# Performance work log

Hardware: AMD Instinct MI355X
Metric: run time of the kernel (lower is better)

## Reference

```python
import jax, jax.numpy as jnp
import numpy as np

GROUPS = 8
HEADS = 8
EPS = 1e-5


def setup_inputs() -> dict:
    key = jax.random.key(0)
    ks = jax.random.split(key, 4)
    B, C, T = 4, 512, 2048
    x = jax.random.normal(ks[0], (B, C, T), dtype=jnp.float32)
    gn_w = jnp.ones((C,), dtype=jnp.float32)
    gn_b = jnp.zeros((C,), dtype=jnp.float32)
    qkv_w = jax.random.normal(ks[1], (3 * C, C), dtype=jnp.float32) * (1.0 / np.sqrt(C))
    qkv_b = jnp.zeros((3 * C,), dtype=jnp.float32)
    proj_w = jax.random.normal(ks[2], (C, C), dtype=jnp.float32) * (1.0 / np.sqrt(C))
    proj_b = jnp.zeros((C,), dtype=jnp.float32)
    return {"x": x, "gn_w": gn_w, "gn_b": gn_b, "qkv_w": qkv_w,
            "qkv_b": qkv_b, "proj_w": proj_w, "proj_b": proj_b}


def reference(x, gn_w, gn_b, qkv_w, qkv_b, proj_w, proj_b):
    b, c, t = x.shape
    # GroupNorm over (channels_in_group, T)
    xg = x.reshape(b, GROUPS, c // GROUPS, t)
    mean = xg.mean(axis=(2, 3), keepdims=True)
    var = xg.var(axis=(2, 3), keepdims=True)
    h = ((xg - mean) * jax.lax.rsqrt(var + EPS)).reshape(b, c, t)
    h = h * gn_w[None, :, None] + gn_b[None, :, None]
    # 1x1 conv qkv: [b, 3c, t]
    qkv = jnp.einsum('oc,bct->bot', qkv_w, h) + qkv_b[None, :, None]
    # split into heads: legacy layout [b*H, 3*ch, t] -> q,k,v each [b*H, ch, t]
    ch = c // HEADS
    qkv = qkv.reshape(b * HEADS, 3 * ch, t)
    q, k, v = qkv[:, :ch], qkv[:, ch:2 * ch], qkv[:, 2 * ch:]
    scale = 1.0 / np.sqrt(np.sqrt(ch))
    weight = jnp.einsum('bct,bcs->bts', q * scale, k * scale)  # [bH, t, t]
    weight = jax.nn.softmax(weight.astype(jnp.float32), axis=-1).astype(q.dtype)
    a = jnp.einsum('bts,bcs->bct', weight, v).reshape(b, c, t)
    # 1x1 conv proj
    out = jnp.einsum('oc,bct->bot', proj_w, a) + proj_b[None, :, None]
    return x + out
```

## Files before the change

### kernel.cpp

```cpp
#include <hip/hip_runtime.h>


typedef __attribute__((ext_vector_type(8))) short short8;
typedef __attribute__((ext_vector_type(4))) float f32x4;
typedef __attribute__((ext_vector_type(16))) float f32x16;

#define T_DIM 2048
#define C_DIM 512
#define B_DIM 4

__device__ __forceinline__ float bf2f(ushort u) {
  union { unsigned int i; float f; } x; x.i = ((unsigned int)u) << 16; return x.f;
}
__device__ __forceinline__ ushort f2bf(float f) {
  union { float f; unsigned int i; } x; x.f = f;
  unsigned int i = x.i;
  return (ushort)((i + 0x7FFFu + ((i >> 16) & 1u)) >> 16);
}
__device__ __forceinline__ unsigned int cvtpk_bf16(float lo, float hi) {
  unsigned int r;
  asm("v_cvt_pk_bf16_f32 %0, %1, %2" : "=v"(r) : "v"(lo), "v"(hi));
  return r;
}
__device__ __forceinline__ float exp2_raw(float x) {
  float r;
  asm("v_exp_f32 %0, %1" : "=v"(r) : "v"(x));
  return r;
}
__device__ __forceinline__ void gl_lds16(const ushort* g, const ushort* l) {
  __builtin_amdgcn_global_load_lds(
      (const __attribute__((address_space(1))) unsigned int*)g,
      (__attribute__((address_space(3))) unsigned int*)l, 16, 0, 0);
}

#define KT_SCALE 0.1803368801f

__global__ __launch_bounds__(256) void prep_kernel(
    const float* __restrict__ qkv_w, ushort* __restrict__ wq,
    const float* __restrict__ proj_w, ushort* __restrict__ wp,
    const float* __restrict__ x, float2* __restrict__ part) {
  const int bi = blockIdx.x;
  const int tid = threadIdx.x;
  if (bi < 1024) {
    const float* s = (bi < 768) ? qkv_w : proj_w;
    ushort* d = (bi < 768) ? wq : wp;
    int i = ((bi < 768) ? bi : bi - 768) * 256 + tid;
    float4 v = ((const float4*)s)[i];
    ushort4 o;
    o.x = f2bf(v.x); o.y = f2bf(v.y); o.z = f2bf(v.z); o.w = f2bf(v.w);
    ((ushort4*)d)[i] = o;
    return;
  }
  const int pb = bi - 1024;
  const float4* p4 = (const float4*)x + (size_t)pb * 2048;
  float s = 0.f, ss = 0.f;
#pragma unroll
  for (int i = 0; i < 8; i++) {
    float4 v = p4[tid + i * 256];
    s += v.x + v.y + v.z + v.w;
    ss += v.x * v.x + v.y * v.y + v.z * v.z + v.w * v.w;
  }
  for (int off = 32; off; off >>= 1) {
    s += __shfl_xor(s, off, 64);
    ss += __shfl_xor(ss, off, 64);
  }
  __shared__ float rbuf[8];
  int w = tid >> 6, lane = tid & 63;
  if (lane == 0) { rbuf[w * 2] = s; rbuf[w * 2 + 1] = ss; }
  __syncthreads();
  if (tid == 0) {
    float S = 0.f, SS = 0.f;
#pragma unroll
    for (int i = 0; i < 4; i++) { S += rbuf[2 * i]; SS += rbuf[2 * i + 1]; }
    part[pb] = make_float2(S, SS);
  }
}

__global__ __launch_bounds__(256) void gn_apply_t_kernel(
    const float* __restrict__ x, const float* __restrict__ gw,
    const float* __restrict__ gb, const float2* __restrict__ part,
    ushort* __restrict__ ht) {
  __shared__ ushort tile[64][66];
  __shared__ float sst[2];
  const int b = blockIdx.z, gy = blockIdx.y, c0 = gy * 64, t0 = blockIdx.x * 64;
  const int tid = threadIdx.x;
  if (tid < 64) {
    float s = 0.f, ss = 0.f;
    if (tid < 16) {
      float2 p = part[(b * 8 + gy) * 16 + tid];
      s = p.x; ss = p.y;
    }
    for (int off = 8; off; off >>= 1) {
      s += __shfl_xor(s, off, 64);
      ss += __shfl_xor(ss, off, 64);
    }
    if (tid == 0) {
      float mean = s * (1.f / 131072.f);
      float var = ss * (1.f / 131072.f) - mean * mean;
      sst[0] = mean;
      sst[1] = rsqrtf(var + 1e-5f);
    }
  }
  __syncthreads();
  const float mean = sst[0], rstd = sst[1];
  {
    const int cc = tid >> 2, tc = (tid & 3) * 16;
    const int c = c0 + cc;
    float sc = rstd * gw[c];
    float bb = gb[c] - mean * sc;
    const float4* src = (const float4*)(x + ((size_t)b * 512 + c) * T_DIM + t0 + tc);
    unsigned int* dst = (unsigned int*)&tile[cc][tc];
#pragma unroll
    for (int q = 0; q < 4; q++) {
      float4 v = src[q];
      float a0 = v.x * sc + bb, a1 = v.y * sc + bb;
      float a2 = v.z * sc + bb, a3 = v.w * sc + bb;
      dst[2 * q] = (unsigned int)f2bf(a0) | ((unsigned int)f2bf(a1) << 16);
      dst[2 * q + 1] = (unsigned int)f2bf(a2) | ((unsigned int)f2bf(a3) << 16);
    }
  }
  __syncthreads();
  {
    const int tt = tid >> 2, ch = (tid & 3) * 16;
    union { uint4 v4[2]; ushort u[16]; } z;
#pragma unroll
    for (int j = 0; j < 16; j++) z.u[j] = tile[ch + j][tt];
    ushort* dst = ht + ((size_t)b * T_DIM + t0 + tt) * 512 + c0 + ch;
    *(uint4*)dst = z.v4[0];
    *(uint4*)(dst + 8) = z.v4[1];
  }
}

template <int MODE, int MF>
__global__ __launch_bounds__(256, 3) void gemm_bt_kernel(
    const ushort* __restrict__ Wb, const ushort* __restrict__ Bt,
    const float* __restrict__ bias, const float* __restrict__ xres,
    ushort* __restrict__ outb, float* __restrict__ outf,
    ushort* __restrict__ ktp, int M) {
  __shared__ ushort As[MF * 32 * 64];
  __shared__ ushort Bs[128 * 64];
  constexpr int NY = (MODE == 0) ? 12 : 8;
  constexpr int CPX = (16 * NY * 4) >> 3;
  const int lin = blockIdx.x + 16 * (blockIdx.y + NY * blockIdx.z);
  const int wl = (lin & 7) * CPX + (lin >> 3);
  const int t0 = (wl & 15) * 128;
  const int rest = wl >> 4;
  const int o0 = (rest % NY) * (MF * 32);
  const int b = rest / NY;
  const int tid = threadIdx.x, lane = tid & 63, w = tid >> 6;
  const int li = lane & 15, g = lane >> 4;
  const int wm = (w >> 1) * (MF * 16), wn = (w & 1) * 64;
  const int r8 = tid >> 3, bl = tid & 7;
  const ushort* Bbase = Bt + (size_t)b * T_DIM * 512;

  f32x4 acc[MF][4];
#pragma unroll
  for (int m = 0; m < MF; m++)
#pragma unroll
    for (int n = 0; n < 4; n++) acc[m][n] = (f32x4){0.f, 0.f, 0.f, 0.f};

  for (int ks = 0; ks < 8; ks++) {
    const int k0 = ks * 64;
#pragma unroll
    for (int i = 0; i < 4; i++) {
      int row = i * 32 + r8;
      int sb = (bl ^ (row & 7)) << 3;
      if (i < MF)
        gl_lds16(Wb + (size_t)(o0 + row) * 512 + k0 + sb, As + row * 64 + bl * 8);
      gl_lds16(Bbase + (size_t)(t0 + row) * 512 + k0 + sb, Bs + row * 64 + bl * 8);
    }
    __syncthreads();
#pragma unroll
    for (int kk = 0; kk < 2; kk++) {
      short8 af[MF], bf[4];
#pragma unroll
      for (int m = 0; m < MF; m++)
        af[m] = *(const short8*)&As[(wm + m * 16 + li) * 64 +
                                    (((kk * 4 + g) ^ (li & 7)) << 3)];
#pragma unroll
      for (int n = 0; n < 4; n++)
        bf[n] = *(const short8*)&Bs[(wn + n * 16 + li) * 64 +
                                    (((kk * 4 + g) ^ (li & 7)) << 3)];
      __builtin_amdgcn_s_setprio(1);
#pragma unroll
      for (int m = 0; m < MF; m++)
#pragma unroll
        for (int n = 0; n < 4; n++)
          acc[m][n] = __builtin_amdgcn_mfma_f32_16x16x32_bf16(af[m], bf[n],
                                                              acc[m][n], 0, 0, 0);
      __builtin_amdgcn_s_setprio(0);
    }
    __syncthreads();
  }

  size_t obase = (size_t)b * M * T_DIM;
#pragma unroll
  for (int m = 0; m < MF; m++) {
    const int om = o0 + wm + m * 16;
    bool isK = false;
    int head = 0, rem0 = 0;
    if (MODE == 0) {
      head = om / 192;
      rem0 = om - head * 192;
      isK = (rem0 >= 64 && rem0 < 128);
    }
    if (MODE == 0 && isK) {
      const int d0 = rem0 - 64 + g * 4;
      const size_t ktbase = (size_t)(b * 8 + head) * T_DIM;
      float bv0 = bias[om + g * 4 + 0];
      float bv1 = bias[om + g * 4 + 1];
      float bv2 = bias[om + g * 4 + 2];
      float bv3 = bias[om + g * 4 + 3];
#pragma unroll
      for (int n = 0; n < 4; n++) {
        int t = t0 + wn + n * 16 + li;
        ushort4 kv;
        kv.x = f2bf(KT_SCALE * (acc[m][n][0] + bv0));
        kv.y = f2bf(KT_SCALE * (acc[m][n][1] + bv1));
        kv.z = f2bf(KT_SCALE * (acc[m][n][2] + bv2));
        kv.w = f2bf(KT_SCALE * (acc[m][n][3] + bv3));
        *(ushort4*)(ktp + (ktbase + t) * 64 + d0) = kv;
      }
    } else {
#pragma unroll
      for (int r = 0; r < 4; r++) {
        int o = om + g * 4 + r;
        float bv = bias[o];
#pragma unroll
        for (int n = 0; n < 4; n++) {
          int t = t0 + wn + n * 16 + li;
          float v = acc[m][n][r] + bv;
          size_t idx = obase + (size_t)o * T_DIM + t;
          if (MODE == 0) outb[idx] = f2bf(v);
          else outf[idx] = v + xres[idx];
        }
      }
    }
  }
}

__global__ __launch_bounds__(256, 4) void attn_part_kernel(
    const ushort* __restrict__ qkv, const ushort* __restrict__ Ktg,
    ushort* __restrict__ opart, float* __restrict__ lpart) {
  __shared__ ushort SH[16384];
  const int bh = blockIdx.x, b = bh >> 3, hh = bh & 7;
  const int ttile = blockIdx.y;
  const int t0 = ttile * 128;
  const int shalf = blockIdx.z;
  const int tid = threadIdx.x, lane = tid & 63, w = tid >> 6;
  const int tl = lane & 31, hi = lane >> 5;
  const size_t base = ((size_t)b * 1536 + hh * 192) * (size_t)T_DIM;
  const ushort* Qp = qkv + base;
  const ushort* Vp = qkv + base + (size_t)128 * T_DIM + shalf * 1024;
  const ushort* Kp = Ktg + (size_t)bh * T_DIM * 64 + (size_t)shalf * 1024 * 64;
  const int tcol = t0 + w * 32 + tl;

  short8 qb[4];
#pragma unroll
  for (int kc = 0; kc < 4; kc++) {
    union { short8 s; ushort u[8]; } tmp;
#pragma unroll
    for (int j = 0; j < 8; j++)
      tmp.u[j] = Qp[(size_t)(kc * 16 + hi * 8 + j) * T_DIM + tcol];
    qb[kc] = tmp.s;
  }

  const int srow = lane >> 3;
  const int sblk = (lane & 7) ^ srow;

  const ushort* kg = Kp + (size_t)(w * 16 + srow) * 64 + sblk * 8;
  const ushort* vg = Vp + (size_t)(w * 16 + srow) * T_DIM + sblk * 8;
  const int ldW = w * 1024;

  f32x16 zv;
#pragma unroll
  for (int r = 0; r < 16; r++) zv[r] = 0.f;
  f32x16 oacc0, oacc1;
#pragma unroll
  for (int r = 0; r < 16; r++) { oacc0[r] = 0.f; oacc1[r] = 0.f; }
  float lsum = 0.f;

  gl_lds16(kg, SH + ldW);
  gl_lds16(kg + 512, SH + ldW + 512);
  gl_lds16(vg, SH + 8192 + ldW);
  gl_lds16(vg + 8 * T_DIM, SH + 8192 + ldW + 512);
  kg += 4096;
  vg += 64;

#define CHUNK(BUF, PF)                                                        \
  {                                                                           \
    __syncthreads();                                                          \
    if (PF) {                                                                 \
      gl_lds16(kg, SH + ((BUF) ^ 1) * 4096 + ldW);                            \
      gl_lds16(kg + 512, SH + ((BUF) ^ 1) * 4096 + ldW + 512);                \
      gl_lds16(vg, SH + 8192 + ((BUF) ^ 1) * 4096 + ldW);                     \
      gl_lds16(vg + 8 * T_DIM, SH + 8192 + ((BUF) ^ 1) * 4096 + ldW + 512);   \
      kg += 4096;                                                             \
      vg += 64;                                                               \
    }                                                                         \
    const ushort* kb = SH + (BUF) * 4096;                                     \
    const ushort* vb = SH + 8192 + (BUF) * 4096;                              \
    f32x16 s0, s1;                                                            \
    __builtin_amdgcn_s_setprio(1);                                            \
    _Pragma("unroll") for (int kc = 0; kc < 4; kc++) {                        \
      const int bo = (((kc * 2 + hi) ^ (tl & 7)) << 3);                       \
      short8 ak0 = *(const short8*)&kb[tl * 64 + bo];                         \
      short8 ak1 = *(const short8*)&kb[(32 + tl) * 64 + bo];                  \
      s0 = __builtin_amdgcn_mfma_f32_32x32x16_bf16(ak0, qb[kc],               \
                                                   kc == 0 ? zv : s0, 0, 0, 0);\
      s1 = __builtin_amdgcn_mfma_f32_32x32x16_bf16(ak1, qb[kc],               \
                                                   kc == 0 ? zv : s1, 0, 0, 0);\
    }                                                                         \
    __builtin_amdgcn_s_setprio(0);                                            \
    _Pragma("unroll") for (int r = 0; r < 16; r++) {                          \
      s0[r] = exp2_raw(s0[r]);                                                \
      s1[r] = exp2_raw(s1[r]);                                                \
    }                                                                         \
    {                                                                         \
      float a0 = (s0[0] + s0[1]) + (s0[2] + s0[3]);                           \
      float a1 = (s0[4] + s0[5]) + (s0[6] + s0[7]);                           \
      float a2 = (s0[8] + s0[9]) + (s0[10] + s0[11]);                         \
      float a3 = (s0[12] + s0[13]) + (s0[14] + s0[15]);                       \
      float b0 = (s1[0] + s1[1]) + (s1[2] + s1[3]);                           \
      float b1 = (s1[4] + s1[5]) + (s1[6] + s1[7]);                           \
      float b2 = (s1[8] + s1[9]) + (s1[10] + s1[11]);                         \
      float b3 = (s1[12] + s1[13]) + (s1[14] + s1[15]);                       \
      lsum += ((a0 + a1) + (a2 + a3)) + ((b0 + b1) + (b2 + b3));              \
    }                                                                         \
    unsigned int pw[2][8];                                                    \
    _Pragma("unroll") for (int p = 0; p < 8; p++) {                           \
      pw[0][p] = cvtpk_bf16(s0[2 * p], s0[2 * p + 1]);                        \
      pw[1][p] = cvtpk_bf16(s1[2 * p], s1[2 * p + 1]);                        \
    }                                                                         \
    short8 bp[4];                                                             \
    _Pragma("unroll") for (int kc = 0; kc < 4; kc++) {                        \
      const int n = kc >> 1, q = (kc & 1) * 4;                                \
      union { short8 s; unsigned int wv[4]; } bu;                             \
      _Pragma("unroll") for (int h = 0; h < 2; h++) {                         \
        unsigned int P0 = pw[n][q + h];                                       \
        unsigned int P1 = pw[n][q + 2 + h];                                   \
        asm volatile("v_permlane32_swap_b32 %0, %1" : "+v"(P0), "+v"(P1));    \
        bu.wv[h] = P0;                                                        \
        bu.wv[2 + h] = P1;                                                    \
      }                                                                       \
      bp[kc] = bu.s;                                                          \
    }                                                                         \
    __builtin_amdgcn_s_setprio(1);                                            \
    _Pragma("unroll") for (int kc = 0; kc < 4; kc++) {                        \
      const int bo = (((kc * 2 + hi) ^ (tl & 7)) << 3);                       \
      short8 av0 = *(const short8*)&vb[tl * 64 + bo];                         \
      short8 av1 = *(const short8*)&vb[(32 + tl) * 64 + bo];                  \
      oacc0 = __builtin_amdgcn_mfma_f32_32x32x16_bf16(av0, bp[kc], oacc0,     \
                                                      0, 0, 0);               \
      oacc1 = __builtin_amdgcn_mfma_f32_32x32x16_bf16(av1, bp[kc], oacc1,     \
                                                      0, 0, 0);               \
    }                                                                         \
    __builtin_amdgcn_s_setprio(0);                                            \
  }

  for (int cc = 0; cc < 8; cc++) {
    CHUNK(0, true);
    CHUNK(1, cc < 7);
  }
#undef CHUNK

  const int pidx = (bh * 16 + ttile) * 2 + shalf;
  ushort* op = opart + (size_t)pidx * 8192;
#pragma unroll
  for (int r = 0; r < 16; r++) {
    int crow = (r & 3) + 8 * (r >> 2) + 4 * hi;
    op[crow * 128 + w * 32 + tl] = f2bf(oacc0[r]);
    op[(32 + crow) * 128 + w * 32 + tl] = f2bf(oacc1[r]);
  }
  float lrow = lsum + __shfl_xor(lsum, 32);
  if (hi == 0) lpart[(size_t)pidx * 128 + w * 32 + tl] = lrow;
}

__global__ __launch_bounds__(256) void combine_kernel(
    const ushort* __restrict__ opart, const float* __restrict__ lpart,
    ushort* __restrict__ at) {
  __shared__ float invl[128];
  __shared__ ushort tile[128][66];
  const int bh = blockIdx.x, ttile = blockIdx.y, b = bh >> 3, hh = bh & 7;
  const int tid = threadIdx.x;
  const size_t pb = (size_t)(bh * 16 + ttile) * 2;
  const float* l0 = lpart + pb * 128;
  if (tid < 128) invl[tid] = 1.f / (l0[tid] + l0[128 + tid]);
  __syncthreads();
  {
    const int c = tid & 63, seg = tid >> 6;
    const ushort* r0 = opart + pb * 8192 + c * 128 + seg * 32;
    union { uint4 v[4]; ushort u[32]; } x0, x1;
#pragma unroll
    for (int j = 0; j < 4; j++) {
      x0.v[j] = *(const uint4*)(r0 + j * 8);
      x1.v[j] = *(const uint4*)(r0 + 8192 + j * 8);
    }
#pragma unroll
    for (int j = 0; j < 32; j++) {
      int t = seg * 32 + j;
      tile[t][c] = f2bf((bf2f(x0.u[j]) + bf2f(x1.u[j])) * invl[t]);
    }
  }
  __syncthreads();
  {
    const int t = tid >> 1, ch = (tid & 1) * 32;
    union { uint4 v[4]; ushort u[32]; } z;
#pragma unroll
    for (int j = 0; j < 32; j++) z.u[j] = tile[t][ch + j];
    uint4* dst = (uint4*)(at + ((size_t)b * T_DIM + ttile * 128 + t) * 512 +
                          hh * 64 + ch);
#pragma unroll
    for (int j = 0; j < 4; j++) dst[j] = z.v[j];
  }
}

extern "C" void kernel_launch(void* const* d_in, const int* in_sizes, int n_in,
                              void* d_out, int out_size, void* d_ws,
                              size_t ws_size, hipStream_t stream) {
  const float* x = (const float*)d_in[0];
  const float* gn_w = (const float*)d_in[1];
  const float* gn_b = (const float*)d_in[2];
  const float* qkv_w = (const float*)d_in[3];
  const float* qkv_b = (const float*)d_in[4];
  const float* proj_w = (const float*)d_in[5];
  const float* proj_b = (const float*)d_in[6];
  float* out = (float*)d_out;

  char* ws = (char*)d_ws;
  float2* part = (float2*)ws;
  ushort* ht_bf = (ushort*)(ws + 8192);
  ushort* at_bf = ht_bf;
  ushort* qkv_bf = (ushort*)(ws + 8192 + 8388608);
  ushort* wq_bf = (ushort*)(ws + 8192 + 8388608 + 25165824);
  ushort* wp_bf = (ushort*)(ws + 8192 + 8388608 + 25165824 + 1572864);
  ushort* kt_bf = (ushort*)(ws + 8192 + 8388608 + 25165824 + 1572864 + 524288);
  ushort* op_bf = (ushort*)(ws + 8192 + 8388608 + 25165824 + 1572864 + 524288 +
                            8388608);
  float* lp_f = (float*)(ws + 8192 + 8388608 + 25165824 + 1572864 + 524288 +
                         8388608 + 16777216);

  prep_kernel<<<1536, 256, 0, stream>>>(qkv_w, wq_bf, proj_w, wp_bf, x, part);
  gn_apply_t_kernel<<<dim3(32, 8, 4), 256, 0, stream>>>(x, gn_w, gn_b, part, ht_bf);
  gemm_bt_kernel<0, 4><<<dim3(16, 12, 4), 256, 0, stream>>>(
      wq_bf, ht_bf, qkv_b, nullptr, qkv_bf, nullptr, kt_bf, 1536);
  attn_part_kernel<<<dim3(32, 16, 2), 256, 0, stream>>>(qkv_bf, kt_bf, op_bf, lp_f);
  combine_kernel<<<dim3(32, 16), 256, 0, stream>>>(op_bf, lp_f, at_bf);
  gemm_bt_kernel<1, 2><<<dim3(16, 8, 4), 256, 0, stream>>>(
      wp_bf, at_bf, proj_b, x, nullptr, out, nullptr, 512);
}
```

Before: 95.41 us.

## Double-buffer GEMM LDS tiles with K=32 stages to overlap loads and MFMA

The qkv/proj GEMM kernel now splits K into 32-wide stages held in two LDS buffers. Each stage's global-to-LDS loads are issued while MFMAs run on the other buffer, instead of load, sync, compute in sequence. It also switches to a rotation-based swizzle with precomputed per-thread source pointers. This doubles the number of barriers and halves the K work between them, which may cost more than the overlap gains.

```diff
diff --git a/kernel.cpp b/kernel.cpp
--- a/kernel.cpp
+++ b/kernel.cpp
@@ -137,10 +137,11 @@
     const float* __restrict__ bias, const float* __restrict__ xres,
     ushort* __restrict__ outb, float* __restrict__ outf,
     ushort* __restrict__ ktp, int M) {
-  __shared__ ushort As[MF * 32 * 64];
-  __shared__ ushort Bs[128 * 64];
+  __shared__ ushort As[2 * MF * 32 * 32];
+  __shared__ ushort Bs[2 * 128 * 32];
   constexpr int NY = (MODE == 0) ? 12 : 8;
   constexpr int CPX = (16 * NY * 4) >> 3;
+  constexpr int ASZ = MF * 32 * 32;
   const int lin = blockIdx.x + 16 * (blockIdx.y + NY * blockIdx.z);
   const int wl = (lin & 7) * CPX + (lin >> 3);
   const int t0 = (wl & 15) * 128;
@@ -150,48 +151,74 @@
   const int tid = threadIdx.x, lane = tid & 63, w = tid >> 6;
   const int li = lane & 15, g = lane >> 4;
   const int wm = (w >> 1) * (MF * 16), wn = (w & 1) * 64;
-  const int r8 = tid >> 3, bl = tid & 7;
   const ushort* Bbase = Bt + (size_t)b * T_DIM * 512;
 
+  const int sro = lane >> 2, slot = lane & 3;
+  const ushort* aW[MF / 2];
+  const ushort* aB[2];
+#pragma unroll
+  for (int j = 0; j < MF / 2; j++) {
+    int row = w * (MF * 8) + j * 16 + sro;
+    int gran = (slot - (row >> 1)) & 3;
+    aW[j] = Wb + (size_t)(o0 + row) * 512 + gran * 8;
+  }
+#pragma unroll
+  for (int j = 0; j < 2; j++) {
+    int row = w * 32 + j * 16 + sro;
+    int gran = (slot - (row >> 1)) & 3;
+    aB[j] = Bbase + (size_t)(t0 + row) * 512 + gran * 8;
+  }
+
   f32x4 acc[MF][4];
 #pragma unroll
   for (int m = 0; m < MF; m++)
 #pragma unroll
     for (int n = 0; n < 4; n++) acc[m][n] = (f32x4){0.f, 0.f, 0.f, 0.f};
 
-  for (int ks = 0; ks < 8; ks++) {
-    const int k0 = ks * 64;
-#pragma unroll
-    for (int i = 0; i < 4; i++) {
-      int row = i * 32 + r8;
-      int sb = (bl ^ (row & 7)) << 3;
-      if (i < MF)
-        gl_lds16(Wb + (size_t)(o0 + row) * 512 + k0 + sb, As + row * 64 + bl * 8);
-      gl_lds16(Bbase + (size_t)(t0 + row) * 512 + k0 + sb, Bs + row * 64 + bl * 8);
-    }
+#define STAGE(BUF, ST)                                                        \
+  {                                                                           \
+    _Pragma("unroll") for (int j = 0; j < MF / 2; j++)                        \
+        gl_lds16(aW[j] + (ST) * 32,                                           \
+                 As + (BUF) * ASZ + (w * (MF * 8) + j * 16) * 32 + lane * 8); \
+    _Pragma("unroll") for (int j = 0; j < 2; j++)                             \
+        gl_lds16(aB[j] + (ST) * 32,                                           \
+                 Bs + (BUF) * 4096 + (w * 32 + j * 16) * 32 + lane * 8);      \
+  }
+
+#define GSTEP(BUF)                                                            \
+  {                                                                           \
+    short8 af[MF], bf[4];                                                     \
+    _Pragma("unroll") for (int m = 0; m < MF; m++) {                          \
+      int r = wm + m * 16 + li;                                               \
+      af[m] = *(const short8*)&As[(BUF) * ASZ + r * 32 +                      \
+                                  (((g + (r >> 1)) & 3) << 3)];               \
+    }                                                                         \
+    _Pragma("unroll") for (int n = 0; n < 4; n++) {                           \
+      int r = wn + n * 16 + li;                                               \
+      bf[n] = *(const short8*)&Bs[(BUF) * 4096 + r * 32 +                     \
+                                  (((g + (r >> 1)) & 3) << 3)];               \
+    }                                                                         \
+    __builtin_amdgcn_s_setprio(1);                                            \
+    _Pragma("unroll") for (int m = 0; m < MF; m++)                            \
+        _Pragma("unroll") for (int n = 0; n < 4; n++)                         \
+            acc[m][n] = __builtin_amdgcn_mfma_f32_16x16x32_bf16(              \
+                af[m], bf[n], acc[m][n], 0, 0, 0);                            \
+    __builtin_amdgcn_s_setprio(0);                                            \
+  }
+
+  STAGE(0, 0);
+#pragma unroll 1
+  for (int s2 = 0; s2 < 8; s2++) {
+    const int st = s2 * 2;
     __syncthreads();
-#pragma unroll
-    for (int kk = 0; kk < 2; kk++) {
-      short8 af[MF], bf[4];
-#pragma unroll
-      for (int m = 0; m < MF; m++)
-        af[m] = *(const short8*)&As[(wm + m * 16 + li) * 64 +
-                                    (((kk * 4 + g) ^ (li & 7)) << 3)];
-#pragma unroll
-      for (int n = 0; n < 4; n++)
-        bf[n] = *(const short8*)&Bs[(wn + n * 16 + li) * 64 +
-                                    (((kk * 4 + g) ^ (li & 7)) << 3)];
-      __builtin_amdgcn_s_setprio(1);
-#pragma unroll
-      for (int m = 0; m < MF; m++)
-#pragma unroll
-        for (int n = 0; n < 4; n++)
-          acc[m][n] = __builtin_amdgcn_mfma_f32_16x16x32_bf16(af[m], bf[n],
-                                                              acc[m][n], 0, 0, 0);
-      __builtin_amdgcn_s_setprio(0);
-    }
+    if (st + 1 < 16) STAGE(1, st + 1);
+    GSTEP(0);
     __syncthreads();
-  }
+    if (st + 2 < 16) STAGE(0, st + 2);
+    GSTEP(1);
+  }
+#undef STAGE
+#undef GSTEP
 
   size_t obase = (size_t)b * M * T_DIM;
 #pragma unroll
```

Measured after the change: 99.57 us. 4.4% more time.
